# Kernel tuning notes

Hardware: AMD Instinct MI355X
Metric: run time of the kernel (lower is better)

## Reference

```python
import jax, jax.numpy as jnp
import numpy as np
import math

B, Q, CQ = 2, 2048, 512
H, D = 8, 64  # no_heads, c_hidden

def setup_inputs() -> dict:
    key = jax.random.key(0)
    ks = jax.random.split(key, 8)
    s = 0.02
    return {
        "q_x": jax.random.normal(ks[0], (B, Q, CQ), jnp.float32),
        "kv_x": jax.random.normal(ks[1], (B, Q, CQ), jnp.float32),
        "bias": jax.random.normal(ks[2], (B, 1, Q, Q), jnp.float32),
        "w_qkv": jax.random.normal(ks[3], (3 * H * D, CQ), jnp.float32) * s,
        "w_o": jax.random.normal(ks[4], (CQ, H * D), jnp.float32) * s,
        "b_o": jnp.zeros((CQ,), jnp.float32),
        "w_g": jax.random.normal(ks[5], (H * D, CQ), jnp.float32) * s,
        "b_g": jnp.zeros((H * D,), jnp.float32),
    }

def reference(q_x, kv_x, bias, w_qkv, w_o, b_o, w_g, b_g):
    # Fused QKV projection from q_x (kv_x is unused by the original module's _prep_qkv)
    qkv = jnp.einsum('bqc,ec->bqe', q_x, w_qkv)  # [B,Q,3*H*D]
    q, k, v = jnp.split(qkv, 3, axis=-1)
    q = q.reshape(B, Q, H, D) / math.sqrt(D)
    k = k.reshape(B, Q, H, D)
    v = v.reshape(B, Q, H, D)
    # scores + additive pairwise bias, softmax over keys
    scores = jnp.einsum('bqhd,bkhd->bhqk', q, k) + bias  # [B,H,Q,K]
    attn = jax.nn.softmax(scores, axis=-1)
    o = jnp.einsum('bhqk,bkhd->bqhd', attn, v)  # [B,Q,H,D]
    # sigmoid gating
    g = jax.nn.sigmoid(jnp.einsum('bqc,ec->bqe', q_x, w_g) + b_g).reshape(B, Q, H, D)
    o = o * g
    # output projection
    o = o.reshape(B, Q, H * D)
    return jnp.einsum('bqe,ce->bqc', o, w_o) + b_o
```

## Files before the change

### kernel.cpp

```cpp
#include <hip/hip_runtime.h>
#include <math.h>

#define B_  2
#define Q_  2048
#define CQ_ 512
#define H_  8
#define D_  64
#define M_  (B_*Q_)
#define L2E 1.44269504088896f

typedef __bf16 bf16;
typedef __bf16 bf16x4 __attribute__((ext_vector_type(4)));
typedef __bf16 bf16x8 __attribute__((ext_vector_type(8)));
typedef float  f32x4  __attribute__((ext_vector_type(4)));
typedef float  f32x16 __attribute__((ext_vector_type(16)));

__device__ __forceinline__ void gl_lds16(const bf16* g, bf16* l) {
    __builtin_amdgcn_global_load_lds(
        (const __attribute__((address_space(1))) unsigned int*)g,
        (__attribute__((address_space(3))) unsigned int*)l, 16, 0, 0);
}

#define S0 (4096*512)
#define S1 (1536*512)
#define S2 (512*512)
#define S3 (512*512)
__global__ __launch_bounds__(256)
void convert_kernel(const float* __restrict__ qx, const float* __restrict__ wqkv,
                    const float* __restrict__ wg, const float* __restrict__ wo,
                    bf16* __restrict__ qxb, bf16* __restrict__ wcat, bf16* __restrict__ wob)
{
    const long long t = (long long)blockIdx.x * 256 + threadIdx.x;
    const long long e = t * 8;
    const float* src; bf16* dst;
    if (e < S0)                { src = qx + e;                  dst = qxb + e; }
    else if (e < S0 + S1)      { src = wqkv + (e - S0);         dst = wcat + (e - S0); }
    else if (e < S0 + S1 + S2) { src = wg + (e - S0 - S1);      dst = wcat + S1 + (e - S0 - S1); }
    else                       { src = wo + (e - S0 - S1 - S2); dst = wob + (e - S0 - S1 - S2); }
    const float4 a = *(const float4*)(src);
    const float4 b = *(const float4*)(src + 4);
    bf16x8 v;
    v[0] = (bf16)a.x; v[1] = (bf16)a.y; v[2] = (bf16)a.z; v[3] = (bf16)a.w;
    v[4] = (bf16)b.x; v[5] = (bf16)b.y; v[6] = (bf16)b.z; v[7] = (bf16)b.w;
    *(bf16x8*)dst = v;
}

template<int BM, int BN, int EPI>
__global__ __launch_bounds__(256)
void gemm_bf16(const bf16* __restrict__ A, const bf16* __restrict__ W,
               const float* __restrict__ bvec, float* __restrict__ fout,
               bf16* __restrict__ qb, bf16* __restrict__ kb, bf16* __restrict__ vb,
               bf16* __restrict__ gb)
{
    constexpr int MI = BM / 32, NJ = BN / 32;
    __shared__ __align__(16) bf16 As[BM * 32];
    __shared__ __align__(16) bf16 Bs[BN * 32];

    const int t = threadIdx.x;
    const int w = t >> 6, lane = t & 63;
    const int l15 = lane & 15, quad = lane >> 4;
    const int wm = w & 1, wn = w >> 1;
    const int bm = blockIdx.x * BM;
    const int bn = blockIdx.y * BN;
    const bool swapped = (EPI == 1) || ((bn >> 9) != 2);

    f32x4 acc[MI][NJ] = {};

    const int rr = t >> 2;
    const int cc = (t & 3) * 8;

    for (int k0 = 0; k0 < 512; k0 += 32) {
        #pragma unroll
        for (int i = 0; i < BM / 64; ++i)
            gl_lds16(A + (size_t)(bm + i * 64 + rr) * 512 + k0 + cc,
                     As + (i * 64 + w * 16) * 32);
        #pragma unroll
        for (int i = 0; i < BN / 64; ++i)
            gl_lds16(W + (size_t)(bn + i * 64 + rr) * 512 + k0 + cc,
                     Bs + (i * 64 + w * 16) * 32);
        __asm__ volatile("s_waitcnt vmcnt(0)" ::: "memory");
        __syncthreads();

        bf16x8 af[MI], bfr[NJ];
        #pragma unroll
        for (int i = 0; i < MI; ++i)
            af[i] = *(const bf16x8*)(As + (wm * (BM / 2) + i * 16 + l15) * 32 + quad * 8);
        #pragma unroll
        for (int j = 0; j < NJ; ++j)
            bfr[j] = *(const bf16x8*)(Bs + (wn * (BN / 2) + j * 16 + l15) * 32 + quad * 8);
        if (swapped) {
            #pragma unroll
            for (int i = 0; i < MI; ++i)
                #pragma unroll
                for (int j = 0; j < NJ; ++j)
                    acc[i][j] = __builtin_amdgcn_mfma_f32_16x16x32_bf16(bfr[j], af[i], acc[i][j], 0, 0, 0);
        } else {
            #pragma unroll
            for (int i = 0; i < MI; ++i)
                #pragma unroll
                for (int j = 0; j < NJ; ++j)
                    acc[i][j] = __builtin_amdgcn_mfma_f32_16x16x32_bf16(af[i], bfr[j], acc[i][j], 0, 0, 0);
        }
        __syncthreads();
    }

    if (swapped) {
        #pragma unroll
        for (int i = 0; i < MI; ++i) {
            const int m = bm + wm * (BM / 2) + i * 16 + l15;
            const int b = m >> 11, qq = m & 2047;
            #pragma unroll
            for (int j = 0; j < NJ; ++j) {
                const int n0 = bn + wn * (BN / 2) + j * 16 + quad * 4;
                const f32x4 cv = acc[i][j];
                if constexpr (EPI == 1) {
                    float4 st;
                    st.x = cv[0] + bvec[n0 + 0];
                    st.y = cv[1] + bvec[n0 + 1];
                    st.z = cv[2] + bvec[n0 + 2];
                    st.w = cv[3] + bvec[n0 + 3];
                    *(float4*)(fout + (size_t)m * 512 + n0) = st;
                } else {
                    const int part = n0 >> 9;
                    if (part == 0) {
                        const int h = (n0 >> 6) & 7, d0 = n0 & 63;
                        bf16x4 q4;
                        #pragma unroll
                        for (int r = 0; r < 4; ++r) q4[r] = (bf16)(cv[r] * (0.125f * L2E));
                        *(bf16x4*)(qb + (size_t)(b * H_ + h) * (Q_ * D_) + (size_t)qq * 64 + d0) = q4;
                    } else if (part == 1) {
                        const int h = (n0 >> 6) & 7, d0 = n0 & 63;
                        const size_t off = (size_t)(b * H_ + h) * (Q_ * D_)
                            + (qq >> 6) * 4096 + ((qq >> 5) & 1) * 2048
                            + (d0 >> 4) * 512 + ((d0 >> 3) & 1) * 256
                            + (qq & 31) * 8 + (d0 & 7);
                        bf16x4 k4;
                        #pragma unroll
                        for (int r = 0; r < 4; ++r) k4[r] = (bf16)cv[r];
                        *(bf16x4*)(kb + off) = k4;
                    } else {
                        const int gcol = n0 & 511;
                        const float4 bv4 = *(const float4*)(bvec + gcol);
                        bf16x4 g4;
                        g4[0] = (bf16)(1.f / (1.f + __expf(-(cv[0] + bv4.x))));
                        g4[1] = (bf16)(1.f / (1.f + __expf(-(cv[1] + bv4.y))));
                        g4[2] = (bf16)(1.f / (1.f + __expf(-(cv[2] + bv4.z))));
                        g4[3] = (bf16)(1.f / (1.f + __expf(-(cv[3] + bv4.w))));
                        *(bf16x4*)(gb + (size_t)m * 512 + gcol) = g4;
                    }
                }
            }
        }
    } else {
        #pragma unroll
        for (int i = 0; i < MI; ++i) {
            const int m0 = bm + wm * (BM / 2) + i * 16 + quad * 4;
            const int b = m0 >> 11, qq0 = m0 & 2047;
            #pragma unroll
            for (int j = 0; j < NJ; ++j) {
                const int n = bn + wn * (BN / 2) + j * 16 + l15;
                const int h = (n >> 6) & 7, d = n & 63;
                const size_t off = (size_t)(b * H_ + h) * (Q_ * D_)
                    + (qq0 >> 6) * 4096 + (d >> 5) * 2048
                    + ((qq0 & 63) >> 4) * 512 + ((qq0 >> 3) & 1) * 256
                    + (d & 31) * 8 + (qq0 & 7);
                bf16x4 v4;
                #pragma unroll
                for (int r = 0; r < 4; ++r) v4[r] = (bf16)acc[i][j][r];
                *(bf16x4*)(vb + off) = v4;
            }
        }
    }
}

__global__ __launch_bounds__(256, 3)
void attn_part(const bf16* __restrict__ qb, const bf16* __restrict__ kf,
               const bf16* __restrict__ vf, const float* __restrict__ bias,
               bf16* __restrict__ po, float2* __restrict__ ml)
{
    __shared__ __align__(16) bf16 Ks[2][4096];
    __shared__ __align__(16) bf16 Vs[2][4096];
    __shared__ __align__(16) bf16 Ps[4][32 * 72];

    const int tid  = threadIdx.x;
    const int wv   = tid >> 6, lane = tid & 63;
    const int l31  = lane & 31, b5 = lane >> 5;
    const int x    = blockIdx.x;
    const int bh   = ((x & 7) << 1) | (x >> 3);
    const int b    = bh >> 3;
    const int qg   = blockIdx.y * 128 + wv * 32 + l31;
    const int ks   = blockIdx.z;

    const bf16* qp = qb + ((size_t)bh * Q_ + qg) * D_;
    bf16x8 bq[4];
    #pragma unroll
    for (int c = 0; c < 4; ++c)
        bq[c] = *(const bf16x8*)(qp + c * 16 + b5 * 8);

    f32x16 acc[2] = {};
    float m_run = -INFINITY, l_run = 0.f;

    const bf16*  kfb  = kf + (size_t)bh * (Q_ * D_) + (size_t)ks * 16 * 4096;
    const bf16*  vfb  = vf + (size_t)bh * (Q_ * D_) + (size_t)ks * 16 * 4096;
    const float* brow = bias + ((size_t)b * Q_ + qg) * Q_ + ks * 1024;

    f32x4 bcur[8], bnxt[8];

    #pragma unroll
    for (int p = 0; p < 2; ++p) {
        gl_lds16(kfb + (wv * 2 + p) * 512 + lane * 8, Ks[0] + (wv * 2 + p) * 512);
        gl_lds16(vfb + (wv * 2 + p) * 512 + lane * 8, Vs[0] + (wv * 2 + p) * 512);
    }
    #pragma unroll
    for (int i = 0; i < 8; ++i)
        bcur[i] = *(const f32x4*)(brow + (i >> 2) * 32 + (i & 3) * 8 + b5 * 4);
    __asm__ volatile("s_waitcnt vmcnt(0)" ::: "memory");
    __syncthreads();

    bf16* pw = Ps[wv] + l31 * 72;

    int cur = 0;
    #pragma unroll 1
    for (int t = 0; t < 16; ++t) {
        if (t < 15) {
            const size_t off = (size_t)(t + 1) * 4096;
            #pragma unroll
            for (int p = 0; p < 2; ++p) {
                gl_lds16(kfb + off + (wv * 2 + p) * 512 + lane * 8,
                         Ks[cur ^ 1] + (wv * 2 + p) * 512);
                gl_lds16(vfb + off + (wv * 2 + p) * 512 + lane * 8,
                         Vs[cur ^ 1] + (wv * 2 + p) * 512);
            }
            const int k0n = (t + 1) * 64;
            #pragma unroll
            for (int i = 0; i < 8; ++i)
                bnxt[i] = *(const f32x4*)(brow + k0n + (i >> 2) * 32 + (i & 3) * 8 + b5 * 4);
        }

        const bf16* Kc = Ks[cur];
        f32x16 sv[2] = {};
        #pragma unroll
        for (int kg = 0; kg < 2; ++kg)
            #pragma unroll
            for (int c = 0; c < 4; ++c) {
                const bf16x8 ak = *(const bf16x8*)(Kc + kg * 2048 + c * 512 + lane * 8);
                sv[kg] = __builtin_amdgcn_mfma_f32_32x32x16_bf16(ak, bq[c], sv[kg], 0, 0, 0);
            }

        float sc[2][16];
        #pragma unroll
        for (int kg = 0; kg < 2; ++kg)
            #pragma unroll
            for (int r = 0; r < 16; ++r)
                sc[kg][r] = fmaf(bcur[kg * 4 + (r >> 2)][r & 3], L2E, sv[kg][r]);

        float tmax = -INFINITY;
        #pragma unroll
        for (int kg = 0; kg < 2; ++kg)
            #pragma unroll
            for (int r = 0; r < 16; ++r)
                tmax = fmaxf(tmax, sc[kg][r]);
        tmax = fmaxf(tmax, __shfl_xor(tmax, 32, 64));

        const float mn = fmaxf(m_run, tmax);
        const float alpha = __builtin_amdgcn_exp2f(m_run - mn);
        m_run = mn;

        float rsum = 0.f;
        #pragma unroll
        for (int kg = 0; kg < 2; ++kg)
            #pragma unroll
            for (int r = 0; r < 16; ++r) {
                sc[kg][r] = __builtin_amdgcn_exp2f(sc[kg][r] - mn);
                rsum += sc[kg][r];
            }
        rsum += __shfl_xor(rsum, 32, 64);
        l_run = l_run * alpha + rsum;
        acc[0] *= alpha;
        acc[1] *= alpha;

        #pragma unroll
        for (int kg = 0; kg < 2; ++kg)
            #pragma unroll
            for (int gi = 0; gi < 4; ++gi) {
                bf16x4 p4;
                p4[0] = (bf16)sc[kg][gi * 4 + 0];
                p4[1] = (bf16)sc[kg][gi * 4 + 1];
                p4[2] = (bf16)sc[kg][gi * 4 + 2];
                p4[3] = (bf16)sc[kg][gi * 4 + 3];
                *(bf16x4*)(pw + kg * 32 + gi * 8 + b5 * 4) = p4;
            }
        __asm__ volatile("s_waitcnt lgkmcnt(0)" ::: "memory");

        const bf16* Vc = Vs[cur];
        #pragma unroll
        for (int c4 = 0; c4 < 4; ++c4) {
            const bf16x8 bp = *(const bf16x8*)(pw + c4 * 16 + b5 * 8);
            #pragma unroll
            for (int dg = 0; dg < 2; ++dg) {
                const bf16x8 av = *(const bf16x8*)(Vc + dg * 2048 + c4 * 512 + lane * 8);
                acc[dg] = __builtin_amdgcn_mfma_f32_32x32x16_bf16(av, bp, acc[dg], 0, 0, 0);
            }
        }

        if (t < 15) {
            #pragma unroll
            for (int i = 0; i < 8; ++i) bcur[i] = bnxt[i];
        }
        __asm__ volatile("s_waitcnt vmcnt(0)" ::: "memory");
        __syncthreads();
        cur ^= 1;
    }

    const float inv = 1.f / l_run;
    const size_t pbase = ((size_t)(ks * 16 + bh) * Q_ + qg) * 64;
    #pragma unroll
    for (int dg = 0; dg < 2; ++dg)
        #pragma unroll
        for (int gi = 0; gi < 4; ++gi) {
            const int d0 = dg * 32 + gi * 8 + b5 * 4;
            bf16x4 ov;
            #pragma unroll
            for (int r = 0; r < 4; ++r)
                ov[r] = (bf16)(acc[dg][gi * 4 + r] * inv);
            *(bf16x4*)(po + pbase + d0) = ov;
        }
    if (b5 == 0)
        ml[(size_t)(ks * 16 + bh) * Q_ + qg] = make_float2(m_run, l_run);
}

__global__ __launch_bounds__(256)
void merge_kernel(const bf16* __restrict__ po, const float2* __restrict__ ml,
                  const bf16* __restrict__ g, bf16* __restrict__ og)
{
    const int gid = blockIdx.x * 256 + threadIdx.x;
    const int row = gid >> 3;
    const int d8  = (gid & 7) * 8;
    const int bh  = row >> 11, qg = row & 2047;
    const int b   = bh >> 3, h = bh & 7;

    const float2 ml0 = ml[row];
    const float2 ml1 = ml[16 * Q_ + row];
    const float  M   = fmaxf(ml0.x, ml1.x);
    const float  w0r = ml0.y * __builtin_amdgcn_exp2f(ml0.x - M);
    const float  w1r = ml1.y * __builtin_amdgcn_exp2f(ml1.x - M);
    const float  inv = 1.f / (w0r + w1r);
    const float  w0 = w0r * inv, w1 = w1r * inv;

    const bf16x8 o0 = *(const bf16x8*)(po + (size_t)row * 64 + d8);
    const bf16x8 o1 = *(const bf16x8*)(po + (size_t)16 * Q_ * 64 + (size_t)row * 64 + d8);
    const size_t obase = ((size_t)(b * Q_ + qg)) * 512 + h * 64 + d8;
    const bf16x8 gv = *(const bf16x8*)(g + obase);
    bf16x8 ov;
    #pragma unroll
    for (int r = 0; r < 8; ++r)
        ov[r] = (bf16)(((float)o0[r] * w0 + (float)o1[r] * w1) * (float)gv[r]);
    *(bf16x8*)(og + obase) = ov;
}

extern "C" void kernel_launch(void* const* d_in, const int* in_sizes, int n_in,
                              void* d_out, int out_size, void* d_ws, size_t ws_size,
                              hipStream_t stream)
{
    const float* q_x   = (const float*)d_in[0];
    const float* bias  = (const float*)d_in[2];
    const float* w_qkv = (const float*)d_in[3];
    const float* w_o   = (const float*)d_in[4];
    const float* b_o   = (const float*)d_in[5];
    const float* w_g   = (const float*)d_in[6];
    const float* b_g   = (const float*)d_in[7];
    float* out = (float*)d_out;

    char* ws = (char*)d_ws;
    bf16*   qxb  = (bf16*)(ws);
    bf16*   wcat = (bf16*)(ws + (4u  << 20));
    bf16*   po   = (bf16*)(ws);
    bf16*   qb   = (bf16*)(ws + (8u  << 20));
    bf16*   kb   = (bf16*)(ws + (12u << 20));
    bf16*   vb   = (bf16*)(ws + (16u << 20));
    bf16*   gb   = (bf16*)(ws + (20u << 20));
    bf16*   ogb  = (bf16*)(ws + (24u << 20));
    bf16*   wob  = (bf16*)(ws + (28u << 20));
    float2* ml   = (float2*)(ws + (28u << 20) + (1u << 19));

    convert_kernel<<<(S0 + S1 + S2 + S3) / (256 * 8), 256, 0, stream>>>(
        q_x, w_qkv, w_g, w_o, qxb, wcat, wob);
    gemm_bf16<128, 128, 0><<<dim3(32, 16), 256, 0, stream>>>(
        qxb, wcat, b_g, nullptr, qb, kb, vb, gb);
    attn_part<<<dim3(B_ * H_, Q_ / 128, 2), 256, 0, stream>>>(qb, kb, vb, bias, po, ml);
    merge_kernel<<<(16 * Q_ * 8) / 256, 256, 0, stream>>>(po, ml, gb, ogb);
    gemm_bf16<64, 128, 1><<<dim3(64, 4), 256, 0, stream>>>(
        ogb, wob, b_o, out, nullptr, nullptr, nullptr, nullptr);
}
```

Measured before the change: 180.3 us.

## Store GEMM operands in k-panel layout for contiguous LDS loads and smaller tiles

The convert and merge kernels now write activations and weights in a 32-wide k-panel layout, so each GEMM k-step loads contiguous 1 KB chunks per wave straight into LDS. Tiles shrink (128x64 and 64x64) to launch more blocks and fill more CUs. The workspace is remapped so buffers can alias. The unconditional bias copy in the attention kernel removes a divergent branch. The risk is that the LDS fragment reads still assume the old row-major tile layout, and the smaller tiles reuse less data per block.

```diff
diff --git a/kernel.cpp b/kernel.cpp
--- a/kernel.cpp
+++ b/kernel.cpp
@@ -33,10 +33,26 @@
     const long long t = (long long)blockIdx.x * 256 + threadIdx.x;
     const long long e = t * 8;
     const float* src; bf16* dst;
-    if (e < S0)                { src = qx + e;                  dst = qxb + e; }
-    else if (e < S0 + S1)      { src = wqkv + (e - S0);         dst = wcat + (e - S0); }
-    else if (e < S0 + S1 + S2) { src = wg + (e - S0 - S1);      dst = wcat + S1 + (e - S0 - S1); }
-    else                       { src = wo + (e - S0 - S1 - S2); dst = wob + (e - S0 - S1 - S2); }
+    if (e < S0) {
+        const int m = (int)(e >> 9), k = (int)(e & 511);
+        src = qx + e;
+        dst = qxb + (size_t)(k >> 5) * (4096 * 32) + (size_t)m * 32 + (k & 31);
+    } else if (e < S0 + S1) {
+        const long long e2 = e - S0;
+        const int n = (int)(e2 >> 9), k = (int)(e2 & 511);
+        src = wqkv + e2;
+        dst = wcat + (size_t)(k >> 5) * (2048 * 32) + (size_t)n * 32 + (k & 31);
+    } else if (e < S0 + S1 + S2) {
+        const long long e2 = e - S0 - S1;
+        const int n = 1536 + (int)(e2 >> 9), k = (int)(e2 & 511);
+        src = wg + e2;
+        dst = wcat + (size_t)(k >> 5) * (2048 * 32) + (size_t)n * 32 + (k & 31);
+    } else {
+        const long long e2 = e - S0 - S1 - S2;
+        const int n = (int)(e2 >> 9), k = (int)(e2 & 511);
+        src = wo + e2;
+        dst = wob + (size_t)(k >> 5) * (512 * 32) + (size_t)n * 32 + (k & 31);
+    }
     const float4 a = *(const float4*)(src);
     const float4 b = *(const float4*)(src + 4);
     bf16x8 v;
@@ -45,7 +61,7 @@
     *(bf16x8*)dst = v;
 }
 
-template<int BM, int BN, int EPI>
+template<int BM, int BN, int EPI, int WNR>
 __global__ __launch_bounds__(256)
 void gemm_bf16(const bf16* __restrict__ A, const bf16* __restrict__ W,
                const float* __restrict__ bvec, float* __restrict__ fout,
@@ -53,6 +69,7 @@
                bf16* __restrict__ gb)
 {
     constexpr int MI = BM / 32, NJ = BN / 32;
+    constexpr int APARTS = BM / 16, BPARTS = BN / 16, NPARTS = APARTS + BPARTS;
     __shared__ __align__(16) bf16 As[BM * 32];
     __shared__ __align__(16) bf16 Bs[BN * 32];
 
@@ -66,18 +83,17 @@
 
     f32x4 acc[MI][NJ] = {};
 
-    const int rr = t >> 2;
-    const int cc = (t & 3) * 8;
-
     for (int k0 = 0; k0 < 512; k0 += 32) {
-        #pragma unroll
-        for (int i = 0; i < BM / 64; ++i)
-            gl_lds16(A + (size_t)(bm + i * 64 + rr) * 512 + k0 + cc,
-                     As + (i * 64 + w * 16) * 32);
-        #pragma unroll
-        for (int i = 0; i < BN / 64; ++i)
-            gl_lds16(W + (size_t)(bn + i * 64 + rr) * 512 + k0 + cc,
-                     Bs + (i * 64 + w * 16) * 32);
+        const size_t apan = (size_t)(k0 >> 5) * (4096 * 32) + (size_t)bm * 32;
+        const size_t bpan = (size_t)(k0 >> 5) * (WNR * 32) + (size_t)bn * 32;
+        #pragma unroll
+        for (int idx = 0; idx < NPARTS / 4; ++idx) {
+            const int p = idx * 4 + w;
+            if (p < APARTS)
+                gl_lds16(A + apan + p * 512 + lane * 8, As + p * 512);
+            else
+                gl_lds16(W + bpan + (p - APARTS) * 512 + lane * 8, Bs + (p - APARTS) * 512);
+        }
         __asm__ volatile("s_waitcnt vmcnt(0)" ::: "memory");
         __syncthreads();
 
@@ -303,10 +319,8 @@
             }
         }
 
-        if (t < 15) {
-            #pragma unroll
-            for (int i = 0; i < 8; ++i) bcur[i] = bnxt[i];
-        }
+        #pragma unroll
+        for (int i = 0; i < 8; ++i) bcur[i] = bnxt[i];
         __asm__ volatile("s_waitcnt vmcnt(0)" ::: "memory");
         __syncthreads();
         cur ^= 1;
@@ -331,7 +345,7 @@
 
 __global__ __launch_bounds__(256)
 void merge_kernel(const bf16* __restrict__ po, const float2* __restrict__ ml,
-                  const bf16* __restrict__ g, bf16* __restrict__ og)
+                  const bf16* __restrict__ g, bf16* __restrict__ ogp)
 {
     const int gid = blockIdx.x * 256 + threadIdx.x;
     const int row = gid >> 3;
@@ -341,21 +355,22 @@
 
     const float2 ml0 = ml[row];
     const float2 ml1 = ml[16 * Q_ + row];
-    const float  M   = fmaxf(ml0.x, ml1.x);
-    const float  w0r = ml0.y * __builtin_amdgcn_exp2f(ml0.x - M);
-    const float  w1r = ml1.y * __builtin_amdgcn_exp2f(ml1.x - M);
+    const float  Mx  = fmaxf(ml0.x, ml1.x);
+    const float  w0r = ml0.y * __builtin_amdgcn_exp2f(ml0.x - Mx);
+    const float  w1r = ml1.y * __builtin_amdgcn_exp2f(ml1.x - Mx);
     const float  inv = 1.f / (w0r + w1r);
     const float  w0 = w0r * inv, w1 = w1r * inv;
 
     const bf16x8 o0 = *(const bf16x8*)(po + (size_t)row * 64 + d8);
     const bf16x8 o1 = *(const bf16x8*)(po + (size_t)16 * Q_ * 64 + (size_t)row * 64 + d8);
-    const size_t obase = ((size_t)(b * Q_ + qg)) * 512 + h * 64 + d8;
-    const bf16x8 gv = *(const bf16x8*)(g + obase);
+    const int m = b * Q_ + qg;
+    const int n = h * 64 + d8;
+    const bf16x8 gv = *(const bf16x8*)(g + (size_t)m * 512 + n);
     bf16x8 ov;
     #pragma unroll
     for (int r = 0; r < 8; ++r)
         ov[r] = (bf16)(((float)o0[r] * w0 + (float)o1[r] * w1) * (float)gv[r]);
-    *(bf16x8*)(og + obase) = ov;
+    *(bf16x8*)(ogp + (size_t)(n >> 5) * (4096 * 32) + (size_t)m * 32 + (n & 31)) = ov;
 }
 
 extern "C" void kernel_launch(void* const* d_in, const int* in_sizes, int n_in,
@@ -372,23 +387,23 @@
     float* out = (float*)d_out;
 
     char* ws = (char*)d_ws;
+    bf16*   po   = (bf16*)(ws);
     bf16*   qxb  = (bf16*)(ws);
     bf16*   wcat = (bf16*)(ws + (4u  << 20));
-    bf16*   po   = (bf16*)(ws);
-    bf16*   qb   = (bf16*)(ws + (8u  << 20));
-    bf16*   kb   = (bf16*)(ws + (12u << 20));
-    bf16*   vb   = (bf16*)(ws + (16u << 20));
-    bf16*   gb   = (bf16*)(ws + (20u << 20));
-    bf16*   ogb  = (bf16*)(ws + (24u << 20));
+    bf16*   qb   = (bf16*)(ws + (12u << 20));
+    bf16*   ogp  = (bf16*)(ws + (12u << 20));
+    bf16*   kb   = (bf16*)(ws + (16u << 20));
+    bf16*   vb   = (bf16*)(ws + (20u << 20));
+    bf16*   gb   = (bf16*)(ws + (24u << 20));
     bf16*   wob  = (bf16*)(ws + (28u << 20));
     float2* ml   = (float2*)(ws + (28u << 20) + (1u << 19));
 
     convert_kernel<<<(S0 + S1 + S2 + S3) / (256 * 8), 256, 0, stream>>>(
         q_x, w_qkv, w_g, w_o, qxb, wcat, wob);
-    gemm_bf16<128, 128, 0><<<dim3(32, 16), 256, 0, stream>>>(
+    gemm_bf16<128, 64, 0, 2048><<<dim3(32, 32), 256, 0, stream>>>(
         qxb, wcat, b_g, nullptr, qb, kb, vb, gb);
     attn_part<<<dim3(B_ * H_, Q_ / 128, 2), 256, 0, stream>>>(qb, kb, vb, bias, po, ml);
-    merge_kernel<<<(16 * Q_ * 8) / 256, 256, 0, stream>>>(po, ml, gb, ogb);
-    gemm_bf16<64, 128, 1><<<dim3(64, 4), 256, 0, stream>>>(
-        ogb, wob, b_o, out, nullptr, nullptr, nullptr, nullptr);
-}
+    merge_kernel<<<(16 * Q_ * 8) / 256, 256, 0, stream>>>(po, ml, gb, ogp);
+    gemm_bf16<64, 64, 1, 512><<<dim3(64, 8), 256, 0, stream>>>(
+        ogp, wob, b_o, out, nullptr, nullptr, nullptr, nullptr);
+}
```

New measurement: 184.7 us. 2.5% more time.
